# Kernel optimization log

Hardware: AMD Instinct MI355X
Metric: run time of the kernel (lower is better)

Reference implementation:

```python
import jax, jax.numpy as jnp
import numpy as np
from jax import lax

B, F, T = 16, 128, 4000
N_RATES = 10
EPS = 1e-05


def setup_inputs() -> dict:
    key = jax.random.key(0)
    k_x, k_s = jax.random.split(key, 2)
    x = jax.random.uniform(k_x, (B, F, T), dtype=jnp.float32)
    means = jnp.array([0.61803, 0.3904, 0.1174, 0.0606, 0.0308,
                       0.0155, 0.0078, 0.0039, 0.002, 0.0001], dtype=jnp.float32)
    # s_k ~ Normal(mean, 0.01*mean); stored as log|s_k|, shape (10, F)
    noise = jax.random.normal(k_s, (N_RATES, F), dtype=jnp.float32)
    s_log = jnp.log(jnp.abs(means[:, None] * (1.0 + 0.01 * noise)))
    alpha_log = jnp.full((F,), jnp.log(jnp.float32(0.8)), dtype=jnp.float32)
    delta_log = jnp.full((F,), jnp.log(jnp.float32(10.0)), dtype=jnp.float32)
    r_log = jnp.full((F,), jnp.log(jnp.float32(0.25)), dtype=jnp.float32)
    return {"x": x, "s_log": s_log, "alpha_log": alpha_log,
            "delta_log": delta_log, "r_log": r_log}


def reference(x, s_log, alpha_log, delta_log, r_log):
    # x: (B, F, T); s_log: (10, F); alpha/delta/r_log: (F,)
    s = jnp.exp(s_log)                      # (10, F)
    alpha = jnp.exp(alpha_log)[:, None]     # (F, 1) -> broadcast over T
    delta = jnp.exp(delta_log)[:, None]
    r = jnp.exp(r_log)[:, None]
    eps = jnp.float32(EPS)

    s_b = s[:, None, :]                     # (10, 1, F)
    init = jnp.broadcast_to(x[..., 0], (N_RATES,) + x.shape[:-1])  # (10, B, F)

    def step(carry, xt):
        # carry: (10, B, F); xt: (B, F)
        carry = (1.0 - s_b) * carry + s_b * xt
        return carry, carry

    xt_seq = jnp.moveaxis(x, -1, 0)         # (T, B, F)
    _, sm = lax.scan(step, init, xt_seq[1:])  # (T-1, 10, B, F)
    smoother = jnp.concatenate([init[None], sm], axis=0)  # (T, 10, B, F)
    smoother = jnp.moveaxis(smoother, 0, -1)               # (10, B, F, T)

    # AGC in log domain: M^(-alpha) computed as exp(-alpha*(log eps + log1p(M/eps)))
    smooth = jnp.exp(-alpha * (jnp.log(eps) + jnp.log1p(smoother / eps)))
    pcen = (x[None] * smooth + delta) ** r - delta ** r    # (10, B, F, T)
    return jnp.transpose(pcen, (1, 0, 2, 3))               # (B, 10, F, T)
```

## Files before the change

### kernel.cpp

```cpp
#include <hip/hip_runtime.h>


typedef float f32x4 __attribute__((ext_vector_type(4)));

constexpr int B_ = 16, F_ = 128, T_ = 4000, R_ = 10;
constexpr float EPS_ = 1e-5f;
constexpr int TPB = 256;
constexpr int WPB = TPB / 64;

__global__ __launch_bounds__(TPB) void pcen_kernel(
    const float* __restrict__ x,
    const float* __restrict__ s_log,
    const float* __restrict__ alpha_log,
    const float* __restrict__ delta_log,
    const float* __restrict__ r_log,
    float* __restrict__ out)
{
    const int wid  = blockIdx.x * WPB + (threadIdx.x >> 6);
    const int lane = threadIdx.x & 63;

    const int b    = wid / (R_ * F_);
    const int rem  = wid - b * (R_ * F_);
    const int rate = rem / F_;
    const int f    = rem - rate * F_;

    const float s     = __builtin_expf(s_log[rate * F_ + f]);
    const float a     = 1.0f - s;
    const float alpha = __builtin_expf(alpha_log[f]);
    const float delta = __builtin_expf(delta_log[f]);
    const float r     = __builtin_expf(r_log[f]);
    const float delta_r = __builtin_exp2f(r * __builtin_log2f(delta));

    const float a2 = a * a, a3 = a2 * a, a4 = a2 * a2;
    const float a8 = a4 * a4, a16 = a8 * a8, a32 = a16 * a16;
    const float a64 = a32 * a32, a128 = a64 * a64, a256 = a128 * a128;

    float pl = 1.0f;
    pl *= (lane & 1)  ? a4   : 1.0f;
    pl *= (lane & 2)  ? a8   : 1.0f;
    pl *= (lane & 4)  ? a16  : 1.0f;
    pl *= (lane & 8)  ? a32  : 1.0f;
    pl *= (lane & 16) ? a64  : 1.0f;
    pl *= (lane & 32) ? a128 : 1.0f;

    const float* xrow = x   + (size_t)(b * F_ + f) * T_;
    float*       orow = out + (size_t)((b * R_ + rate) * F_ + f) * T_;

    float carry = xrow[0];

    auto pcen1 = [&](float xv, float m) -> float {
        const float sm = __builtin_exp2f(-alpha * __builtin_log2f(EPS_ + m));
        return __builtin_exp2f(r * __builtin_log2f(fmaf(xv, sm, delta))) - delta_r;
    };

    for (int t0 = 0; t0 < T_; t0 += 512) {
        const int tA = t0 + lane * 4;
        const int tB = tA + 256;
        const bool actA = (tA < T_);
        const bool actB = (tB < T_);
        float4 vA = make_float4(0.f, 0.f, 0.f, 0.f);
        float4 vB = make_float4(0.f, 0.f, 0.f, 0.f);
        if (actA) vA = *reinterpret_cast<const float4*>(xrow + tA);
        if (actB) vB = *reinterpret_cast<const float4*>(xrow + tB);

        const float lA0 = s * vA.x;
        const float lA1 = fmaf(a, lA0, s * vA.y);
        const float lA2 = fmaf(a, lA1, s * vA.z);
        const float lA3 = fmaf(a, lA2, s * vA.w);
        const float lB0 = s * vB.x;
        const float lB1 = fmaf(a, lB0, s * vB.y);
        const float lB2 = fmaf(a, lB1, s * vB.z);
        const float lB3 = fmaf(a, lB2, s * vB.w);

        float YA = lA3;
        if (lane == 0) YA = fmaf(a4, carry, YA);
        float YB = lB3;

        float uA, uB;
        uA = __shfl_up(YA, 1);  uB = __shfl_up(YB, 1);
        if (lane >= 1)  { YA = fmaf(a4,   uA, YA); YB = fmaf(a4,   uB, YB); }
        uA = __shfl_up(YA, 2);  uB = __shfl_up(YB, 2);
        if (lane >= 2)  { YA = fmaf(a8,   uA, YA); YB = fmaf(a8,   uB, YB); }
        uA = __shfl_up(YA, 4);  uB = __shfl_up(YB, 4);
        if (lane >= 4)  { YA = fmaf(a16,  uA, YA); YB = fmaf(a16,  uB, YB); }
        uA = __shfl_up(YA, 8);  uB = __shfl_up(YB, 8);
        if (lane >= 8)  { YA = fmaf(a32,  uA, YA); YB = fmaf(a32,  uB, YB); }
        uA = __shfl_up(YA, 16); uB = __shfl_up(YB, 16);
        if (lane >= 16) { YA = fmaf(a64,  uA, YA); YB = fmaf(a64,  uB, YB); }
        uA = __shfl_up(YA, 32); uB = __shfl_up(YB, 32);
        if (lane >= 32) { YA = fmaf(a128, uA, YA); YB = fmaf(a128, uB, YB); }

        float yinA = __shfl_up(YA, 1);
        if (lane == 0) yinA = carry;
        float yinB = __shfl_up(YB, 1);
        if (lane == 0) yinB = 0.0f;
        const float exitA = __shfl(YA, 63);
        yinB = fmaf(pl, exitA, yinB);
        carry = fmaf(a256, exitA, __shfl(YB, 63));

        if (actA) {
            const float mA0 = fmaf(a,  yinA, lA0);
            const float mA1 = fmaf(a2, yinA, lA1);
            const float mA2 = fmaf(a3, yinA, lA2);
            const float mA3 = fmaf(a4, yinA, lA3);
            f32x4 o;
            o.x = pcen1(vA.x, mA0);
            o.y = pcen1(vA.y, mA1);
            o.z = pcen1(vA.z, mA2);
            o.w = pcen1(vA.w, mA3);
            __builtin_nontemporal_store(o, reinterpret_cast<f32x4*>(orow + tA));
        }
        if (actB) {
            const float mB0 = fmaf(a,  yinB, lB0);
            const float mB1 = fmaf(a2, yinB, lB1);
            const float mB2 = fmaf(a3, yinB, lB2);
            const float mB3 = fmaf(a4, yinB, lB3);
            f32x4 o;
            o.x = pcen1(vB.x, mB0);
            o.y = pcen1(vB.y, mB1);
            o.z = pcen1(vB.z, mB2);
            o.w = pcen1(vB.w, mB3);
            __builtin_nontemporal_store(o, reinterpret_cast<f32x4*>(orow + tB));
        }
    }
}

extern "C" void kernel_launch(void* const* d_in, const int* in_sizes, int n_in,
                              void* d_out, int out_size, void* d_ws, size_t ws_size,
                              hipStream_t stream) {
    const float* x         = (const float*)d_in[0];
    const float* s_log     = (const float*)d_in[1];
    const float* alpha_log = (const float*)d_in[2];
    const float* delta_log = (const float*)d_in[3];
    const float* r_log     = (const float*)d_in[4];
    float* out = (float*)d_out;

    const int n_waves = B_ * R_ * F_;
    const int blocks  = n_waves / WPB;
    pcen_kernel<<<blocks, TPB, 0, stream>>>(x, s_log, alpha_log, delta_log, r_log, out);
}
```

Before: 91.50 us.

## Share x row across all ten rates via double-buffered LDS in one block

Each block now handles one (batch, feature) row with ten waves, one per rate, instead of four unrelated waves. The first two waves stage each 512-sample chunk of x into a double-buffered shared-memory tile that all rate waves read. This is meant to cut repeated global or cache reads of x, which was previously loaded ten times. In exchange it adds a block-wide barrier per chunk, which couples the waves, and uses larger 640-thread blocks.

```diff
diff --git a/kernel.cpp b/kernel.cpp
--- a/kernel.cpp
+++ b/kernel.cpp
@@ -5,8 +5,8 @@
 
 constexpr int B_ = 16, F_ = 128, T_ = 4000, R_ = 10;
 constexpr float EPS_ = 1e-5f;
-constexpr int TPB = 256;
-constexpr int WPB = TPB / 64;
+constexpr int TPB = 64 * R_;
+constexpr int NCHUNK = (T_ + 511) / 512;
 
 __global__ __launch_bounds__(TPB) void pcen_kernel(
     const float* __restrict__ x,
@@ -16,13 +16,13 @@
     const float* __restrict__ r_log,
     float* __restrict__ out)
 {
-    const int wid  = blockIdx.x * WPB + (threadIdx.x >> 6);
+    __shared__ float lds[2][512];
+
     const int lane = threadIdx.x & 63;
+    const int rate = threadIdx.x >> 6;
 
-    const int b    = wid / (R_ * F_);
-    const int rem  = wid - b * (R_ * F_);
-    const int rate = rem / F_;
-    const int f    = rem - rate * F_;
+    const int b = blockIdx.x / F_;
+    const int f = blockIdx.x - b * F_;
 
     const float s     = __builtin_expf(s_log[rate * F_ + f]);
     const float a     = 1.0f - s;
@@ -48,20 +48,32 @@
 
     float carry = xrow[0];
 
+    auto stage = [&](int k, int buf) {
+        if (threadIdx.x < 128) {
+            const int t = k * 512 + threadIdx.x * 4;
+            float4 v = make_float4(0.f, 0.f, 0.f, 0.f);
+            if (t < T_) v = *reinterpret_cast<const float4*>(xrow + t);
+            *reinterpret_cast<float4*>(&lds[buf][threadIdx.x * 4]) = v;
+        }
+    };
+
     auto pcen1 = [&](float xv, float m) -> float {
         const float sm = __builtin_exp2f(-alpha * __builtin_log2f(EPS_ + m));
         return __builtin_exp2f(r * __builtin_log2f(fmaf(xv, sm, delta))) - delta_r;
     };
 
-    for (int t0 = 0; t0 < T_; t0 += 512) {
-        const int tA = t0 + lane * 4;
+    stage(0, 0);
+    __syncthreads();
+
+    for (int k = 0; k < NCHUNK; ++k) {
+        if (k + 1 < NCHUNK) stage(k + 1, (k + 1) & 1);
+
+        const float* Lb = lds[k & 1];
+        const float4 vA = *reinterpret_cast<const float4*>(Lb + lane * 4);
+        const float4 vB = *reinterpret_cast<const float4*>(Lb + 256 + lane * 4);
+
+        const int tA = k * 512 + lane * 4;
         const int tB = tA + 256;
-        const bool actA = (tA < T_);
-        const bool actB = (tB < T_);
-        float4 vA = make_float4(0.f, 0.f, 0.f, 0.f);
-        float4 vB = make_float4(0.f, 0.f, 0.f, 0.f);
-        if (actA) vA = *reinterpret_cast<const float4*>(xrow + tA);
-        if (actB) vB = *reinterpret_cast<const float4*>(xrow + tB);
 
         const float lA0 = s * vA.x;
         const float lA1 = fmaf(a, lA0, s * vA.y);
@@ -98,7 +110,7 @@
         yinB = fmaf(pl, exitA, yinB);
         carry = fmaf(a256, exitA, __shfl(YB, 63));
 
-        if (actA) {
+        if (tA < T_) {
             const float mA0 = fmaf(a,  yinA, lA0);
             const float mA1 = fmaf(a2, yinA, lA1);
             const float mA2 = fmaf(a3, yinA, lA2);
@@ -110,7 +122,7 @@
             o.w = pcen1(vA.w, mA3);
             __builtin_nontemporal_store(o, reinterpret_cast<f32x4*>(orow + tA));
         }
-        if (actB) {
+        if (tB < T_) {
             const float mB0 = fmaf(a,  yinB, lB0);
             const float mB1 = fmaf(a2, yinB, lB1);
             const float mB2 = fmaf(a3, yinB, lB2);
@@ -122,6 +134,8 @@
             o.w = pcen1(vB.w, mB3);
             __builtin_nontemporal_store(o, reinterpret_cast<f32x4*>(orow + tB));
         }
+
+        __syncthreads();
     }
 }
 
@@ -135,7 +149,6 @@
     const float* r_log     = (const float*)d_in[4];
     float* out = (float*)d_out;
 
-    const int n_waves = B_ * R_ * F_;
-    const int blocks  = n_waves / WPB;
+    const int blocks = B_ * F_;
     pcen_kernel<<<blocks, TPB, 0, stream>>>(x, s_log, alpha_log, delta_log, r_log, out);
 }
```

Measured after the change: 108.7 us. 1.19x slower.
